# Performance work log

Hardware: AMD Instinct MI355X
Metric: run time of the kernel (lower is better)

## Reference

```python
import jax, jax.numpy as jnp
import numpy as np

B, LS, LT = 64, 64, 64
E, H = 512, 512
VS, VT = 32000, 32000


def setup_inputs() -> dict:
    key = jax.random.key(0)
    ks = jax.random.split(key, 16)
    s = 0.02
    inp = {
        "src": jax.random.randint(ks[0], (B, LS), 0, VS),
        "tgt": jax.random.randint(ks[1], (B, LT), 0, VT),
        # encoder params
        "src_embed": jax.random.normal(ks[2], (VS, E), jnp.float32) * s,
        "enc_Wx": jax.random.normal(ks[3], (E, 4 * H), jnp.float32) * s,   # [i|f|g|o]
        "enc_Wh": jax.random.normal(ks[4], (H, 4 * H), jnp.float32) * s,
        "enc_b": jnp.zeros((4 * H,), jnp.float32),
        # decoder params
        "tgt_embed": jax.random.normal(ks[5], (VT, E), jnp.float32) * s,
        "att_Wh": jax.random.normal(ks[6], (H, H), jnp.float32) * s,
        "att_Ws": jax.random.normal(ks[7], (H, H), jnp.float32) * s,
        "att_v": jax.random.normal(ks[8], (H,), jnp.float32) * s,
        "dec_Wx": jax.random.normal(ks[9], (E + H, 4 * H), jnp.float32) * s,
        "dec_Wh": jax.random.normal(ks[10], (H, 4 * H), jnp.float32) * s,
        "dec_b": jnp.zeros((4 * H,), jnp.float32),
        "h2o_W": jax.random.normal(ks[11], (2 * H, VT), jnp.float32) * s,
        "h2o_b": jnp.zeros((VT,), jnp.float32),
    }
    return inp


def _lstm_step(x, h, c, Wx, Wh, b):
    # x:(B,in), h,c:(B,H). Gates packed as [i|f|g|o] along last dim (same math
    # as 8 separate nn.Linear calls with biases summed).
    z = x @ Wx + h @ Wh + b
    i, f, g, o = jnp.split(z, 4, axis=-1)
    c_new = jax.nn.sigmoid(f) * c + jax.nn.sigmoid(i) * jnp.tanh(g)
    h_new = jax.nn.sigmoid(o) * jnp.tanh(c_new)
    return h_new, c_new


def reference(src, tgt, src_embed, enc_Wx, enc_Wh, enc_b, tgt_embed,
              att_Wh, att_Ws, att_v, dec_Wx, dec_Wh, dec_b, h2o_W, h2o_b):
    Bs = src.shape[0]
    h0 = jnp.zeros((Bs, H), jnp.float32)
    c0 = jnp.zeros((Bs, H), jnp.float32)

    # ---- encoder: scan over source timesteps ----
    src_emb = src_embed[src]                       # (B,Ls,E)
    xs_enc = jnp.swapaxes(src_emb, 0, 1)           # (Ls,B,E)

    def enc_step(carry, x):
        h, c = carry
        h, c = _lstm_step(x, h, c, enc_Wx, enc_Wh, enc_b)
        return (h, c), h

    (h_enc, c_enc), enc_hs = jax.lax.scan(enc_step, (h0, c0), xs_enc)
    enc_hiddens = jnp.swapaxes(enc_hs, 0, 1)       # (B,Ls,H)

    # encoder-side attention projection is decoder-state independent: hoist it
    enc_t = enc_hiddens @ att_Wh                   # (B,Ls,H)

    # ---- decoder: teacher forcing, scan over target timesteps ----
    tgt_emb = tgt_embed[tgt]                       # (B,Lt,E)
    xs_dec = jnp.swapaxes(tgt_emb, 0, 1)           # (Lt,B,E)

    def dec_step(carry, emb):
        h, c = carry
        # Bahdanau additive attention on previous decoder hidden h
        dec_t = h @ att_Ws                                        # (B,H)
        energy = jnp.tanh(enc_t + dec_t[:, None, :]) @ att_v      # (B,Ls)
        attn = jax.nn.softmax(energy, axis=-1)                    # (B,Ls)
        context = jnp.einsum('bs,bsh->bh', attn, enc_hiddens)     # (B,H)
        lstm_in = jnp.concatenate([emb, context], axis=-1)        # (B,E+H)
        h, c = _lstm_step(lstm_in, h, c, dec_Wx, dec_Wh, dec_b)
        logits = jnp.concatenate([h, context], axis=-1) @ h2o_W + h2o_b
        out = jax.nn.log_softmax(logits, axis=-1)                 # (B,Vt)
        return (h, c), out

    _, outs = jax.lax.scan(dec_step, (h_enc, c_enc), xs_dec)      # (Lt,B,Vt)
    return jnp.swapaxes(outs, 0, 1)                               # (B,Lt,Vt)
```

## Files before the change

kernel.cpp:

```cpp
#include <hip/hip_runtime.h>
#include <hip/hip_bf16.h>
#include <math.h>

#define BB 64
#define LL 64
#define EE 512
#define HH 512
#define G4 2048
#define VT 32000
#define RT 4096

typedef unsigned short u16;
typedef unsigned int u32;
typedef unsigned char u8;
typedef __attribute__((ext_vector_type(2))) unsigned int u32x2;
typedef __attribute__((ext_vector_type(8))) unsigned short ushort8;
typedef __attribute__((ext_vector_type(8))) short bf16x8;
typedef __attribute__((ext_vector_type(4))) float f32x4;

__device__ u16   gW2T[(size_t)VT * 1024];
__device__ u16   gEncWxT[G4 * EE];
__device__ u16   gEncWhT[G4 * HH];
__device__ u16   gAttWhT[HH * HH];
__device__ u16   gDecWxTe[G4 * EE];
__device__ u16   gDecWxTc[G4 * HH];
__device__ u16   gDecWhT[G4 * HH];
__device__ u8    gWs8[HH * HH];
__device__ u16   gSrcEmb[RT * EE];
__device__ u16   gTgtEmb[RT * EE];
__device__ float gXWxE[(size_t)RT * G4];
__device__ float gXWxD[(size_t)RT * G4];
__device__ u16   gEncHb[(size_t)RT * HH];
__device__ u16   gEncHb2[(size_t)RT * HH];
__device__ u16   gEncTb[(size_t)RT * HH];
__device__ u16   gHcat[(size_t)RT * 1024];
__device__ float gC[BB * HH];
__device__ float gAv[HH];
__device__ unsigned gFlagE[64];
__device__ unsigned gFlagB[64];
__device__ unsigned gFlagC[64];
__device__ unsigned gStep;

__device__ __forceinline__ u16 f2b(float f) {
    union { float f; unsigned u; } v{f};
    unsigned r = v.u + 0x7fffu + ((v.u >> 16) & 1u);
    return (u16)(r >> 16);
}
__device__ __forceinline__ float b2f(u16 x) {
    union { unsigned u; float f; } v; v.u = ((unsigned)x) << 16; return v.f;
}
__device__ __forceinline__ float sigm(float x) { return 1.f / (1.f + __expf(-x)); }
__device__ __forceinline__ float ftanh(float x) {
    x = fminf(15.f, fmaxf(-15.f, x));
    float e = __expf(2.f * x);
    return (e - 1.f) / (e + 1.f);
}

__device__ unsigned char encf8(float f) {
    union { float f; unsigned u; } v{f};
    unsigned s = (v.u >> 31) << 7;
    float af = fabsf(f);
    if (af < 0.0009765625f) return (unsigned char)s;
    if (af >= 448.f) return (unsigned char)(s | 0x7E);
    if (af < 0.015625f) {
        int q = (int)rintf(af * 512.f);
        if (q >= 8) return (unsigned char)(s | 0x08);
        return (unsigned char)(s | q);
    }
    int e; float m = frexpf(af, &e);
    int E = e - 1 + 7;
    int q = (int)rintf((m * 2.f - 1.f) * 8.f);
    if (q == 8) { E++; q = 0; }
    if (E >= 15) return (unsigned char)(s | 0x7E);
    return (unsigned char)(s | (E << 3) | q);
}
__device__ __forceinline__ float decf8s(unsigned v) {
    unsigned s = v >> 7, e = (v >> 3) & 15, m = v & 7;
    float mag = e ? ldexpf((float)(8 + m), (int)e - 10) : ldexpf((float)m, -9);
    return s ? -mag : mag;
}
#if __has_builtin(__builtin_amdgcn_cvt_f32_fp8)
#define DEC8(w, sel) __builtin_amdgcn_cvt_f32_fp8((int)(w), sel)
#else
#define DEC8(w, sel) decf8s(((w) >> (8 * (sel))) & 0xFFu)
#endif

__device__ __forceinline__ void ld16(const void* addr, bf16x8* a) {
    asm volatile(
        "global_load_dwordx4 %0, %16, off sc0 sc1\n\t"
        "global_load_dwordx4 %1, %16, off offset:64 sc0 sc1\n\t"
        "global_load_dwordx4 %2, %16, off offset:128 sc0 sc1\n\t"
        "global_load_dwordx4 %3, %16, off offset:192 sc0 sc1\n\t"
        "global_load_dwordx4 %4, %16, off offset:256 sc0 sc1\n\t"
        "global_load_dwordx4 %5, %16, off offset:320 sc0 sc1\n\t"
        "global_load_dwordx4 %6, %16, off offset:384 sc0 sc1\n\t"
        "global_load_dwordx4 %7, %16, off offset:448 sc0 sc1\n\t"
        "global_load_dwordx4 %8, %16, off offset:512 sc0 sc1\n\t"
        "global_load_dwordx4 %9, %16, off offset:576 sc0 sc1\n\t"
        "global_load_dwordx4 %10, %16, off offset:640 sc0 sc1\n\t"
        "global_load_dwordx4 %11, %16, off offset:704 sc0 sc1\n\t"
        "global_load_dwordx4 %12, %16, off offset:768 sc0 sc1\n\t"
        "global_load_dwordx4 %13, %16, off offset:832 sc0 sc1\n\t"
        "global_load_dwordx4 %14, %16, off offset:896 sc0 sc1\n\t"
        "global_load_dwordx4 %15, %16, off offset:960 sc0 sc1\n\t"
        "s_waitcnt vmcnt(0)"
        : "=&v"(a[0]), "=&v"(a[1]), "=&v"(a[2]), "=&v"(a[3]),
          "=&v"(a[4]), "=&v"(a[5]), "=&v"(a[6]), "=&v"(a[7]),
          "=&v"(a[8]), "=&v"(a[9]), "=&v"(a[10]), "=&v"(a[11]),
          "=&v"(a[12]), "=&v"(a[13]), "=&v"(a[14]), "=&v"(a[15])
        : "v"(addr) : "memory");
}
__device__ __forceinline__ u32 ld1(const void* addr) {
    u32 r;
    asm volatile("global_load_dword %0, %1, off sc0 sc1\n\ts_waitcnt vmcnt(0)"
                 : "=&v"(r) : "v"(addr) : "memory");
    return r;
}
__device__ __forceinline__ void st8b(void* p, u32x2 v) {
    asm volatile("global_store_dwordx2 %0, %1, off sc0 sc1" :: "v"(p), "v"(v) : "memory");
}
__device__ __forceinline__ void st32b(u32* p, u32 v) {
    asm volatile("global_store_dword %0, %1, off sc0 sc1" :: "v"(p), "v"(v) : "memory");
}

__device__ __forceinline__ void setflag(unsigned* f, unsigned v) {
    asm volatile("s_waitcnt vmcnt(0)" ::: "memory");
    __syncthreads();
    if (threadIdx.x == 0) st32b((u32*)f, v);
}
__device__ __forceinline__ void waitflags(unsigned* flags, int n, unsigned target) {
    if (threadIdx.x < 64) {
        const unsigned* p = flags + (threadIdx.x & (n - 1));
        for (;;) {
            u32 v = ld1(p);
            if (__all(v >= target)) break;
            __builtin_amdgcn_s_sleep(1);
        }
    }
    __syncthreads();
}

__device__ __forceinline__ void g2l16(const u16* g, u16* l) {
    __builtin_amdgcn_global_load_lds(
        (const __attribute__((address_space(1))) unsigned int*)g,
        (__attribute__((address_space(3))) unsigned int*)l, 16, 0, 0);
}
__device__ __forceinline__ void g2l16nt(const u16* g, u16* l) {
    __builtin_amdgcn_global_load_lds(
        (const __attribute__((address_space(1))) unsigned int*)g,
        (__attribute__((address_space(3))) unsigned int*)l, 16, 0, 2);
}

__device__ inline u16* bf16sel(int s) {
    switch (s) {
        case 1: return gEncWxT; case 2: return gEncWhT;
        case 3: return gAttWhT; case 4: return gDecWxTe; case 5: return gDecWxTc;
        default: return gDecWhT;
    }
}

__global__ __launch_bounds__(256) void k_transpose(const float* __restrict__ in, int R, int C, int sel) {
    __shared__ float tile[32][33];
    int tx = threadIdx.x & 31, ty0 = threadIdx.x >> 5;
    int c0 = blockIdx.x * 32, r0 = blockIdx.y * 32;
#pragma unroll
    for (int k = 0; k < 4; k++) {
        int ty = ty0 + k * 8;
        tile[ty][tx] = in[(size_t)(r0 + ty) * C + c0 + tx];
    }
    __syncthreads();
    u16* out = bf16sel(sel);
#pragma unroll
    for (int k = 0; k < 4; k++) {
        int ty = ty0 + k * 8;
        out[(size_t)(c0 + ty) * R + r0 + tx] = f2b(tile[tx][ty]);
    }
}

__global__ __launch_bounds__(256) void k_tofp8(const float* __restrict__ in) {
    int i = blockIdx.x * 256 + threadIdx.x;
    gWs8[i] = encf8(in[i]);
}

__global__ __launch_bounds__(256) void k_gather(const int* __restrict__ tok, const float* __restrict__ tab, int sel) {
    int r = blockIdx.x;
    int b = r & 63, t = r >> 6;
    int token = tok[b * LL + t];
    u16* dst = (sel == 0) ? gSrcEmb : gTgtEmb;
    const float* srow = tab + (size_t)token * EE;
    for (int e = threadIdx.x; e < EE; e += 256)
        dst[(size_t)r * EE + e] = f2b(srow[e]);
}

__global__ __launch_bounds__(256) void k_zero() {
    int i = blockIdx.x * 256 + threadIdx.x;
    gC[i] = 0.f;
    if (i < 64) st32b((u32*)(gFlagE + i), 0u);
}

__global__ __launch_bounds__(256) void k_rst(const float* __restrict__ av) {
    int t = threadIdx.x;
    gAv[t] = av[t];
    gAv[t + 256] = av[t + 256];
    if (t < 64) {
        st32b((u32*)(gFlagB + t), 0u);
        st32b((u32*)(gFlagC + t), 0u);
    }
    if (t == 0) st32b((u32*)&gStep, 0u);
}

__global__ __launch_bounds__(256) void k_gemm(int selA, int lda, int selB, int ldb,
                                              int M, int N, int K, int epi,
                                              const float* __restrict__ bias, int selOut) {
    __shared__ u16 sA[128 * 72];
    __shared__ u16 sB[128 * 72];
    const u16* Ag = (selA == 0) ? gSrcEmb : gEncHb;
    const u16* Bg = (selB == 0) ? gEncWxT : gAttWhT;
    float* Cg = gXWxE;

    int tid = threadIdx.x, l = tid & 63, wid = tid >> 6, wr = wid >> 1, wc = wid & 1;
    int ar = l & 15, ak = (l >> 4) * 8;
    int rowM = blockIdx.y * 128, colN = blockIdx.x * 128;
    f32x4 acc[4][4];
#pragma unroll
    for (int m = 0; m < 4; m++)
#pragma unroll
        for (int n = 0; n < 4; n++) acc[m][n] = (f32x4){0.f, 0.f, 0.f, 0.f};

    for (int k0 = 0; k0 < K; k0 += 64) {
#pragma unroll
        for (int it = 0; it < 4; it++) {
            int idx = it * 256 + tid;
            int row = idx >> 3, cc = idx & 7;
            *(ushort8*)(sA + row * 72 + cc * 8) =
                *(const ushort8*)(Ag + (size_t)(rowM + row) * lda + k0 + cc * 8);
            *(ushort8*)(sB + row * 72 + cc * 8) =
                *(const ushort8*)(Bg + (size_t)(colN + row) * ldb + k0 + cc * 8);
        }
        __syncthreads();
#pragma unroll
        for (int ks = 0; ks < 2; ks++) {
            bf16x8 a[4], b[4];
#pragma unroll
            for (int m = 0; m < 4; m++) a[m] = *(const bf16x8*)(sA + (wr * 64 + m * 16 + ar) * 72 + ks * 32 + ak);
#pragma unroll
            for (int n = 0; n < 4; n++) b[n] = *(const bf16x8*)(sB + (wc * 64 + n * 16 + ar) * 72 + ks * 32 + ak);
#pragma unroll
            for (int m = 0; m < 4; m++)
#pragma unroll
                for (int n = 0; n < 4; n++)
                    acc[m][n] = __builtin_amdgcn_mfma_f32_16x16x32_bf16(a[m], b[n], acc[m][n], 0, 0, 0);
        }
        __syncthreads();
    }
    int rb = (l >> 4) * 4;
#pragma unroll
    for (int m = 0; m < 4; m++)
#pragma unroll
        for (int n = 0; n < 4; n++)
#pragma unroll
            for (int ri = 0; ri < 4; ri++) {
                int row = rowM + wr * 64 + m * 16 + rb + ri;
                int col = colN + wc * 64 + n * 16 + ar;
                float v = acc[m][n][ri];
                if (epi == 2) Cg[(size_t)row * N + col] = v + bias[col];
                else gEncTb[(size_t)((row & 63) * 64 + (row >> 6)) * N + col] = f2b(v);
            }
}

__global__ __launch_bounds__(256) void k_encoder(const float* __restrict__ dec_b,
                                                 const float* __restrict__ h2o_W) {
    __shared__ char smem[67584];
    int tid = threadIdx.x, l = tid & 63, wid = tid >> 6;
    int bx = blockIdx.x;
    int ar = l & 15, ak = (l >> 4) * 8, rb = (l >> 4) * 4;
    if (bx < 32) {
        u16* sW = (u16*)smem;
        u16* s_hout = (u16*)(smem + 65536);
        int j = bx;
#pragma unroll
        for (int it = 0; it < 16; it++) {
            int idx = it * 256 + tid;
            int lr = idx >> 6, kc = idx & 63;
            int gcol = (lr >> 4) * 512 + j * 16 + (lr & 15);
            int off = (lr * 1024 + kc * 16) ^ ((lr & 7) << 4);
            *(ushort8*)((char*)sW + off) = *(const ushort8*)(gEncWhT + (size_t)gcol * 512 + kc * 8);
        }
        __syncthreads();
        int arow = wid * 16 + ar, aoff = (l >> 4) * 16;
        int hcol = j * 16 + ar;
        for (int t = 0; t < LL; t++) {
            float xwv[4][4];
#pragma unroll
            for (int ri = 0; ri < 4; ri++) {
                const float* xw = gXWxE + (size_t)(t * BB + wid * 16 + rb + ri) * G4;
#pragma unroll
                for (int g = 0; g < 4; g++) xwv[ri][g] = xw[g * 512 + hcol];
            }
            f32x4 acc[4];
#pragma unroll
            for (int g = 0; g < 4; g++) acc[g] = (f32x4){0.f, 0.f, 0.f, 0.f};
            if (t > 0) {
                waitflags(gFlagE, 32, (unsigned)t);
                bf16x8 af[16];
                ld16((const char*)gEncHb + (size_t)((t - 1) * BB + arow) * 1024 + aoff, af);
#pragma unroll
                for (int kk = 0; kk < 16; kk++) {
                    int k = kk * 32 + ak;
#pragma unroll
                    for (int g = 0; g < 4; g++) {
                        int lr = g * 16 + ar;
                        bf16x8 b = *(const bf16x8*)((char*)sW + ((lr * 1024 + k * 2) ^ ((lr & 7) << 4)));
                        acc[g] = __builtin_amdgcn_mfma_f32_16x16x32_bf16(af[kk], b, acc[g], 0, 0, 0);
                    }
                }
            }
#pragma unroll
            for (int ri = 0; ri < 4; ri++) {
                int row = wid * 16 + rb + ri;
                float zi = acc[0][ri] + xwv[ri][0];
                float zf = acc[1][ri] + xwv[ri][1];
                float zg = acc[2][ri] + xwv[ri][2];
                float zo = acc[3][ri] + xwv[ri][3];
                float co = gC[row * HH + hcol];
                float cn = sigm(zf) * co + sigm(zi) * ftanh(zg);
                float hn = sigm(zo) * ftanh(cn);
                gC[row * HH + hcol] = cn;
                s_hout[row * 16 + ar] = f2b(hn);
            }
            __syncthreads();
            {
                int row = tid >> 2, seg = tid & 3;
                u32x2 v = *(const u32x2*)(s_hout + row * 16 + seg * 4);
                st8b(gEncHb + (size_t)(t * BB + row) * HH + j * 16 + seg * 4, v);
                *(u32x2*)(gEncHb2 + (size_t)(row * LL + t) * HH + j * 16 + seg * 4) = v;
            }
            setflag(gFlagE + j, (unsigned)(t + 1));
        }
    } else if (bx < 96) {
        u16* sA = (u16*)smem;
        u16* sB = (u16*)(smem + 18432);
        int wr = wid >> 1, wc = wid & 1;
        for (int it8 = 0; it8 < 8; it8++) {
            int ti = (bx - 32) * 8 + it8;
            int bxx = ti & 15, byy = ti >> 4;
            int rowM = byy * 128, colN = bxx * 128;
            f32x4 acc[4][4];
#pragma unroll
            for (int m = 0; m < 4; m++)
#pragma unroll
                for (int n = 0; n < 4; n++) acc[m][n] = (f32x4){0.f, 0.f, 0.f, 0.f};
            for (int k0 = 0; k0 < 512; k0 += 64) {
#pragma unroll
                for (int it = 0; it < 4; it++) {
                    int idx = it * 256 + tid;
                    int row = idx >> 3, cc = idx & 7;
                    *(ushort8*)(sA + row * 72 + cc * 8) =
                        *(const ushort8*)(gTgtEmb + (size_t)(rowM + row) * 512 + k0 + cc * 8);
                    *(ushort8*)(sB + row * 72 + cc * 8) =
                        *(const ushort8*)(gDecWxTe + (size_t)(colN + row) * 512 + k0 + cc * 8);
                }
                __syncthreads();
#pragma unroll
                for (int ks = 0; ks < 2; ks++) {
                    bf16x8 a[4], b[4];
#pragma unroll
                    for (int m = 0; m < 4; m++) a[m] = *(const bf16x8*)(sA + (wr * 64 + m * 16 + ar) * 72 + ks * 32 + ak);
#pragma unroll
                    for (int n = 0; n < 4; n++) b[n] = *(const bf16x8*)(sB + (wc * 64 + n * 16 + ar) * 72 + ks * 32 + ak);
#pragma unroll
                    for (int m = 0; m < 4; m++)
#pragma unroll
                        for (int n = 0; n < 4; n++)
                            acc[m][n] = __builtin_amdgcn_mfma_f32_16x16x32_bf16(a[m], b[n], acc[m][n], 0, 0, 0);
                }
                __syncthreads();
            }
#pragma unroll
            for (int m = 0; m < 4; m++)
#pragma unroll
                for (int n = 0; n < 4; n++)
#pragma unroll
                    for (int ri = 0; ri < 4; ri++) {
                        int row = rowM + wr * 64 + m * 16 + rb + ri;
                        int col = colN + wc * 64 + n * 16 + ar;
                        gXWxD[(size_t)row * G4 + col] = acc[m][n][ri] + dec_b[col];
                    }
        }
    } else {
        float (*tile)[33] = (float(*)[33])smem;
        int tx = tid & 31, ty0 = tid >> 5;
        for (int k = 0; k < 200; k++) {
            int ti = (bx - 96) * 200 + k;
            int ct = ti % 1000, rt = ti / 1000;
            int c0 = ct * 32, r0 = rt * 32;
            __syncthreads();
#pragma unroll
            for (int kk = 0; kk < 4; kk++) {
                int ty = ty0 + kk * 8;
                tile[ty][tx] = h2o_W[(size_t)(r0 + ty) * VT + c0 + tx];
            }
            __syncthreads();
#pragma unroll
            for (int kk = 0; kk < 4; kk++) {
                int ty = ty0 + kk * 8;
                gW2T[(size_t)(c0 + ty) * 1024 + r0 + tx] = f2b(tile[tx][ty]);
            }
        }
    }
}

__global__ __launch_bounds__(256) void k_decoder(const float* __restrict__ h2o_b,
                                                 float* __restrict__ out) {
    __shared__ u16 sWh[64 * 512];
    __shared__ u16 sWx[64 * 512];
    __shared__ u16 s_hout[64 * 16];
    __shared__ float s_h[512];
    __shared__ float s_dt[512];
    __shared__ float s_av[512];
    __shared__ float s_att[64];
    __shared__ float s_red[256];
    __shared__ float s_mv[4][520];
    int tid = threadIdx.x, l = tid & 63, wid = tid >> 6;
    int bx = blockIdx.x;
    int ar = l & 15, ak = (l >> 4) * 8, rb = (l >> 4) * 4;
    int arow = wid * 16 + ar, aoff = (l >> 4) * 16;
    if (bx >= 96) {
        u16* csA = sWh;
        u16* csB = sWh + 128 * 64;
        int wr = wid >> 1, wc = wid & 1;
        int srow = wid * 32 + (l >> 3);
        int scol = (l & 7) * 8;
        int ci = bx - 96;
        for (int jt = 0; jt < 50; jt++) {
            int T = ci + 160 * jt;
            int byy = T / 250, bxx = T % 250;
            unsigned tgt = (unsigned)(2 * byy + 2);
            if (tid == 0) {
                while (ld1(&gStep) < tgt) __builtin_amdgcn_s_sleep(32);
            }
            __syncthreads();
            int rowM = byy * 128, colN = bxx * 128;
            f32x4 acc[4][4];
#pragma unroll
            for (int m = 0; m < 4; m++)
#pragma unroll
                for (int n = 0; n < 4; n++) acc[m][n] = (f32x4){0.f, 0.f, 0.f, 0.f};
            for (int k0 = 0; k0 < 1024; k0 += 64) {
#pragma unroll
                for (int c = 0; c < 4; c++) {
                    int r = srow + c * 8;
                    g2l16(gHcat + (size_t)(rowM + r) * 1024 + k0 + scol, csA + r * 64 + scol);
                    g2l16nt(gW2T + (size_t)(colN + r) * 1024 + k0 + scol, csB + r * 64 + scol);
                }
                __syncthreads();
#pragma unroll
                for (int ks = 0; ks < 2; ks++) {
                    bf16x8 a[4], b[4];
#pragma unroll
                    for (int m = 0; m < 4; m++) a[m] = *(const bf16x8*)(csA + (wr * 64 + m * 16 + ar) * 64 + ks * 32 + ak);
#pragma unroll
                    for (int n = 0; n < 4; n++) b[n] = *(const bf16x8*)(csB + (wc * 64 + n * 16 + ar) * 64 + ks * 32 + ak);
#pragma unroll
                    for (int m = 0; m < 4; m++)
#pragma unroll
                        for (int n = 0; n < 4; n++)
                            acc[m][n] = __builtin_amdgcn_mfma_f32_16x16x32_bf16(a[m], b[n], acc[m][n], 0, 0, 0);
                }
                __syncthreads();
            }
#pragma unroll
            for (int m = 0; m < 4; m++)
#pragma unroll
                for (int n = 0; n < 4; n++)
#pragma unroll
                    for (int ri = 0; ri < 4; ri++) {
                        int row = rowM + wr * 64 + m * 16 + rb + ri;
                        int col = colN + wc * 64 + n * 16 + ar;
                        out[(size_t)((row & 63) * 64 + (row >> 6)) * VT + col] = acc[m][n][ri] + h2o_b[col];
                    }
        }
        return;
    }
    if (bx >= 64) {
        int j = bx - 64;
#pragma unroll
        for (int it = 0; it < 16; it++) {
            int idx = it * 256 + tid;
            int lr = idx >> 6, kc = idx & 63;
            int gcol = (lr >> 4) * 512 + j * 16 + (lr & 15);
            int off = (lr * 1024 + kc * 16) ^ ((lr & 7) << 4);
            *(ushort8*)((char*)sWh + off) = *(const ushort8*)(gDecWhT + (size_t)gcol * 512 + kc * 8);
            *(ushort8*)((char*)sWx + off) = *(const ushort8*)(gDecWxTc + (size_t)gcol * 512 + kc * 8);
        }
    } else {
        s_av[tid] = gAv[tid];
        s_av[tid + 256] = gAv[tid + 256];
    }
    __syncthreads();
    for (int t = 0; t < LL; t++) {
        if (bx >= 64) {
            int j = bx - 64;
            int hcol = j * 16 + ar;
            float xwv[4][4];
#pragma unroll
            for (int ri = 0; ri < 4; ri++) {
                const float* xw = gXWxD + (size_t)(t * BB + wid * 16 + rb + ri) * G4;
#pragma unroll
                for (int g = 0; g < 4; g++) xwv[ri][g] = xw[g * 512 + hcol];
            }
            if (t > 0) waitflags(gFlagC, 32, (unsigned)t);
            if (t > 0 && bx == 64 && tid == 0) st32b((u32*)&gStep, (unsigned)t);
            bf16x8 af[16];
            const char* baseA = (t == 0)
                ? ((const char*)gEncHb + (size_t)(63 * BB + arow) * 1024 + aoff)
                : ((const char*)gHcat + (size_t)((t - 1) * BB + arow) * 2048 + aoff);
            ld16(baseA, af);
            f32x4 acc[4];
#pragma unroll
            for (int g = 0; g < 4; g++) acc[g] = (f32x4){0.f, 0.f, 0.f, 0.f};
#pragma unroll
            for (int kk = 0; kk < 16; kk++) {
                int k = kk * 32 + ak;
#pragma unroll
                for (int g = 0; g < 4; g++) {
                    int lr = g * 16 + ar;
                    bf16x8 b = *(const bf16x8*)((char*)sWh + ((lr * 1024 + k * 2) ^ ((lr & 7) << 4)));
                    acc[g] = __builtin_amdgcn_mfma_f32_16x16x32_bf16(af[kk], b, acc[g], 0, 0, 0);
                }
            }
            waitflags(gFlagB, 64, (unsigned)(t + 1));
            bf16x8 cf[16];
            ld16((const char*)gHcat + (size_t)(t * BB + arow) * 2048 + 1024 + aoff, cf);
#pragma unroll
            for (int kk = 0; kk < 16; kk++) {
                int k = kk * 32 + ak;
#pragma unroll
                for (int g = 0; g < 4; g++) {
                    int lr = g * 16 + ar;
                    bf16x8 b = *(const bf16x8*)((char*)sWx + ((lr * 1024 + k * 2) ^ ((lr & 7) << 4)));
                    acc[g] = __builtin_amdgcn_mfma_f32_16x16x32_bf16(cf[kk], b, acc[g], 0, 0, 0);
                }
            }
#pragma unroll
            for (int ri = 0; ri < 4; ri++) {
                int row = wid * 16 + rb + ri;
                float zi = acc[0][ri] + xwv[ri][0];
                float zf = acc[1][ri] + xwv[ri][1];
                float zg = acc[2][ri] + xwv[ri][2];
                float zo = acc[3][ri] + xwv[ri][3];
                float co = gC[row * HH + hcol];
                float cn = sigm(zf) * co + sigm(zi) * ftanh(zg);
                float hn = sigm(zo) * ftanh(cn);
                gC[row * HH + hcol] = cn;
                s_hout[row * 16 + ar] = f2b(hn);
            }
            __syncthreads();
            {
                int row = tid >> 2, seg = tid & 3;
                u32x2 v = *(const u32x2*)(s_hout + row * 16 + seg * 4);
                st8b(gHcat + (size_t)(t * BB + row) * 1024 + j * 16 + seg * 4, v);
            }
            setflag(gFlagC + j, (unsigned)(t + 1));
        } else {
            int b = bx;
            if (t > 0) waitflags(gFlagC, 32, (unsigned)t);
            const char* hb = (t == 0) ? ((const char*)gEncHb + (size_t)(63 * BB + b) * 1024)
                                      : ((const char*)gHcat + (size_t)((t - 1) * BB + b) * 2048);
            u32 hw = ld1(hb + 4 * tid);
            s_h[2 * tid] = b2f((u16)(hw & 0xffff));
            s_h[2 * tid + 1] = b2f((u16)(hw >> 16));
            __syncthreads();
            {
                int c8 = tid & 63, kq = tid >> 6;
                float a8[8];
#pragma unroll
                for (int jj = 0; jj < 8; jj++) a8[jj] = 0.f;
                const u8* wp = gWs8 + (size_t)(kq * 128) * 512 + c8 * 8;
#pragma unroll 4
                for (int i = 0; i < 128; i++) {
                    u32x2 w = *(const u32x2*)(wp + (size_t)i * 512);
                    float hk = s_h[kq * 128 + i];
                    a8[0] += hk * DEC8(w.x, 0);
                    a8[1] += hk * DEC8(w.x, 1);
                    a8[2] += hk * DEC8(w.x, 2);
                    a8[3] += hk * DEC8(w.x, 3);
                    a8[4] += hk * DEC8(w.y, 0);
                    a8[5] += hk * DEC8(w.y, 1);
                    a8[6] += hk * DEC8(w.y, 2);
                    a8[7] += hk * DEC8(w.y, 3);
                }
#pragma unroll
                for (int jj = 0; jj < 8; jj++) s_mv[kq][c8 * 8 + jj] = a8[jj];
            }
            __syncthreads();
            s_dt[tid] = s_mv[0][tid] + s_mv[1][tid] + s_mv[2][tid] + s_mv[3][tid];
            s_dt[tid + 256] = s_mv[0][tid + 256] + s_mv[1][tid + 256] + s_mv[2][tid + 256] + s_mv[3][tid + 256];
            __syncthreads();
            {
                int s = tid >> 2, q = tid & 3;
                const u16* et = gEncTb + (size_t)(b * 64 + s) * 512 + q * 128;
                const float* dtp = s_dt + q * 128;
                const float* avp = s_av + q * 128;
                float p = 0.f;
#pragma unroll
                for (int i = 0; i < 16; i++) {
                    ushort8 ev = *(const ushort8*)(et + i * 8);
#pragma unroll
                    for (int jj = 0; jj < 8; jj++) {
                        int h = i * 8 + jj;
                        p += ftanh(b2f((u16)ev[jj]) + dtp[h]) * avp[h];
                    }
                }
                s_red[tid] = p;
            }
            __syncthreads();
            if (tid < 64) {
                float v = s_red[tid * 4] + s_red[tid * 4 + 1] + s_red[tid * 4 + 2] + s_red[tid * 4 + 3];
                float m = v;
                for (int o = 32; o; o >>= 1) m = fmaxf(m, __shfl_xor(m, o));
                float e = __expf(v - m);
                float ss = e;
                for (int o = 32; o; o >>= 1) ss += __shfl_xor(ss, o);
                s_att[tid] = e / ss;
            }
            __syncthreads();
            int c = tid * 2;
            float c0 = 0.f, c1 = 0.f;
            const u16* eh = gEncHb2 + (size_t)b * LL * HH;
#pragma unroll 8
            for (int s2 = 0; s2 < 64; s2++) {
                float a = s_att[s2];
                u32 w = *(const u32*)(eh + (size_t)s2 * HH + c);
                c0 += a * b2f((u16)(w & 0xffff));
                c1 += a * b2f((u16)(w >> 16));
            }
            u32 cw = (u32)f2b(c0) | ((u32)f2b(c1) << 16);
            st32b((u32*)(gHcat + (size_t)(t * BB + b) * 1024 + 512 + c), cw);
            setflag(gFlagB + b, (unsigned)(t + 1));
        }
    }
    if (bx == 64) {
        waitflags(gFlagC, 32, 64u);
        waitflags(gFlagB, 64, 64u);
        if (tid == 0) st32b((u32*)&gStep, 64u);
    }
}

__global__ __launch_bounds__(256) void k_lsm(float* __restrict__ out) {
    int row = blockIdx.x, tid = threadIdx.x;
    float4* p4 = (float4*)(out + (size_t)row * VT);
    float m = -1e30f, s = 0.f;
    for (int i = tid; i < VT / 4; i += 256) {
        float4 v = p4[i];
        float mx = fmaxf(fmaxf(v.x, v.y), fmaxf(v.z, v.w));
        float mn = fmaxf(m, mx);
        s = s * __expf(m - mn) + __expf(v.x - mn) + __expf(v.y - mn) + __expf(v.z - mn) + __expf(v.w - mn);
        m = mn;
    }
    for (int o = 32; o; o >>= 1) {
        float m2 = __shfl_xor(m, o), s2 = __shfl_xor(s, o);
        float mn = fmaxf(m, m2);
        s = s * __expf(m - mn) + s2 * __expf(m2 - mn);
        m = mn;
    }
    __shared__ float rm[4], rs[4];
    if ((tid & 63) == 0) { rm[tid >> 6] = m; rs[tid >> 6] = s; }
    __syncthreads();
    float mm = fmaxf(fmaxf(rm[0], rm[1]), fmaxf(rm[2], rm[3]));
    float ss = rs[0] * __expf(rm[0] - mm) + rs[1] * __expf(rm[1] - mm) +
               rs[2] * __expf(rm[2] - mm) + rs[3] * __expf(rm[3] - mm);
    float lse = mm + __logf(ss);
    for (int i = tid; i < VT / 4; i += 256) {
        float4 v = p4[i];
        v.x -= lse; v.y -= lse; v.z -= lse; v.w -= lse;
        p4[i] = v;
    }
}

extern "C" void kernel_launch(void* const* d_in, const int* in_sizes, int n_in,
                              void* d_out, int out_size, void* d_ws, size_t ws_size,
                              hipStream_t stream) {
    const int*   src       = (const int*)d_in[0];
    const int*   tgt       = (const int*)d_in[1];
    const float* src_embed = (const float*)d_in[2];
    const float* enc_Wx    = (const float*)d_in[3];
    const float* enc_Wh    = (const float*)d_in[4];
    const float* enc_b     = (const float*)d_in[5];
    const float* tgt_embed = (const float*)d_in[6];
    const float* att_Wh    = (const float*)d_in[7];
    const float* att_Ws    = (const float*)d_in[8];
    const float* att_v     = (const float*)d_in[9];
    const float* dec_Wx    = (const float*)d_in[10];
    const float* dec_Wh    = (const float*)d_in[11];
    const float* dec_b     = (const float*)d_in[12];
    const float* h2o_W     = (const float*)d_in[13];
    const float* h2o_b     = (const float*)d_in[14];
    float* out = (float*)d_out;
    dim3 blk(256);

    k_transpose<<<dim3(G4 / 32, EE / 32), blk, 0, stream>>>(enc_Wx, EE, G4, 1);
    k_transpose<<<dim3(G4 / 32, HH / 32), blk, 0, stream>>>(enc_Wh, HH, G4, 2);
    k_transpose<<<dim3(HH / 32, HH / 32), blk, 0, stream>>>(att_Wh, HH, HH, 3);
    k_transpose<<<dim3(G4 / 32, EE / 32), blk, 0, stream>>>(dec_Wx, EE, G4, 4);
    k_transpose<<<dim3(G4 / 32, HH / 32), blk, 0, stream>>>(dec_Wx + (size_t)512 * G4, HH, G4, 5);
    k_transpose<<<dim3(G4 / 32, HH / 32), blk, 0, stream>>>(dec_Wh, HH, G4, 6);
    k_tofp8<<<HH * HH / 256, blk, 0, stream>>>(att_Ws);
    k_gather<<<RT, blk, 0, stream>>>(src, src_embed, 0);
    k_gather<<<RT, blk, 0, stream>>>(tgt, tgt_embed, 1);
    k_zero<<<128, blk, 0, stream>>>();
    k_gemm<<<dim3(G4 / 128, RT / 128), blk, 0, stream>>>(0, 512, 0, 512, RT, G4, 512, 2, enc_b, 0);
    const float* decb = dec_b;
    const float* h2ow = h2o_W;
    void* eargs[] = { (void*)&decb, (void*)&h2ow };
    hipLaunchCooperativeKernel((const void*)k_encoder, dim3(256), dim3(256), eargs, 0, stream);
    k_gemm<<<dim3(HH / 128, RT / 128), blk, 0, stream>>>(2, 512, 2, 512, RT, HH, 512, 4, nullptr, 2);
    k_rst<<<1, blk, 0, stream>>>(att_v);
    const float* h2ob = h2o_b;
    float* outp = out;
    void* dargs[] = { (void*)&h2ob, (void*)&outp };
    hipLaunchCooperativeKernel((const void*)k_decoder, dim3(256), dim3(256), dargs, 0, stream);
    k_lsm<<<RT, blk, 0, stream>>>(out);
}
```

Measured before the change: 2.774 ms.

## Split decoder recurrence into two independent batch halves with separate flag groups

The decoder LSTM blocks are split into two groups of 32, each handling 32 batch rows, so the two batch halves proceed independently, each with its own flags and step counter. Gate results go through shared memory so every thread computes two cells. Attention blocks wait only on their own half's flags. The output GEMM now uses 128 blocks instead of 160 and waits on both step counters. The aim is to shorten the per-step critical path through narrower synchronization, at the cost of fewer GEMM workers and more flag traffic.

```diff
diff --git a/kernel.cpp b/kernel.cpp
--- a/kernel.cpp
+++ b/kernel.cpp
@@ -40,6 +40,7 @@
 __device__ unsigned gFlagB[64];
 __device__ unsigned gFlagC[64];
 __device__ unsigned gStep;
+__device__ unsigned gStep2;
 
 __device__ __forceinline__ u16 f2b(float f) {
     union { float f; unsigned u; } v{f};
@@ -206,7 +207,7 @@
         st32b((u32*)(gFlagB + t), 0u);
         st32b((u32*)(gFlagC + t), 0u);
     }
-    if (t == 0) st32b((u32*)&gStep, 0u);
+    if (t == 0) { st32b((u32*)&gStep, 0u); st32b((u32*)&gStep2, 0u); }
 }
 
 __global__ __launch_bounds__(256) void k_gemm(int selA, int lda, int selB, int ldb,
@@ -414,7 +415,8 @@
                                                  float* __restrict__ out) {
     __shared__ u16 sWh[64 * 512];
     __shared__ u16 sWx[64 * 512];
-    __shared__ u16 s_hout[64 * 16];
+    __shared__ float s_z[4][32][17];
+    __shared__ u16 s_hout[32 * 16];
     __shared__ float s_h[512];
     __shared__ float s_dt[512];
     __shared__ float s_av[512];
@@ -424,20 +426,22 @@
     int tid = threadIdx.x, l = tid & 63, wid = tid >> 6;
     int bx = blockIdx.x;
     int ar = l & 15, ak = (l >> 4) * 8, rb = (l >> 4) * 4;
-    int arow = wid * 16 + ar, aoff = (l >> 4) * 16;
-    if (bx >= 96) {
+    int aoff = (l >> 4) * 16;
+    if (bx >= 128) {
         u16* csA = sWh;
         u16* csB = sWh + 128 * 64;
         int wr = wid >> 1, wc = wid & 1;
         int srow = wid * 32 + (l >> 3);
         int scol = (l & 7) * 8;
-        int ci = bx - 96;
-        for (int jt = 0; jt < 50; jt++) {
-            int T = ci + 160 * jt;
+        int ci = bx - 128;
+        for (int jt = 0; jt < 63; jt++) {
+            int T = ci + 128 * jt;
+            if (T >= 8000) break;
             int byy = T / 250, bxx = T % 250;
             unsigned tgt = (unsigned)(2 * byy + 2);
             if (tid == 0) {
                 while (ld1(&gStep) < tgt) __builtin_amdgcn_s_sleep(32);
+                while (ld1(&gStep2) < tgt) __builtin_amdgcn_s_sleep(32);
             }
             __syncthreads();
             int rowM = byy * 128, colN = bxx * 128;
@@ -483,7 +487,8 @@
         return;
     }
     if (bx >= 64) {
-        int j = bx - 64;
+        int c = (bx - 64) >> 5, j = (bx - 64) & 31, cb = 32 * c;
+        int mt = wid & 1, gp = wid >> 1;
 #pragma unroll
         for (int it = 0; it < 16; it++) {
             int idx = it * 256 + tid;
@@ -493,80 +498,105 @@
             *(ushort8*)((char*)sWh + off) = *(const ushort8*)(gDecWhT + (size_t)gcol * 512 + kc * 8);
             *(ushort8*)((char*)sWx + off) = *(const ushort8*)(gDecWxTc + (size_t)gcol * 512 + kc * 8);
         }
-    } else {
+        __syncthreads();
+        int cell0 = tid, cell1 = tid + 256;
+        int r30 = cell0 >> 4, hc0 = cell0 & 15;
+        int r31 = cell1 >> 4, hc1 = cell1 & 15;
+        int arow2 = cb + mt * 16 + ar;
+        for (int t = 0; t < LL; t++) {
+            float xwv[2][4];
+            const float* xw0 = gXWxD + (size_t)(t * 64 + cb + r30) * G4;
+            const float* xw1 = gXWxD + (size_t)(t * 64 + cb + r31) * G4;
+#pragma unroll
+            for (int g = 0; g < 4; g++) {
+                xwv[0][g] = xw0[g * 512 + 16 * j + hc0];
+                xwv[1][g] = xw1[g * 512 + 16 * j + hc1];
+            }
+            if (t > 0) waitflags(gFlagC + cb, 32, (unsigned)t);
+            if (t > 0 && j == 0 && tid == 0)
+                st32b(c ? (u32*)&gStep2 : (u32*)&gStep, (unsigned)t);
+            bf16x8 af[16];
+            const char* baseA = (t == 0)
+                ? ((const char*)gEncHb + (size_t)(63 * 64 + arow2) * 1024 + aoff)
+                : ((const char*)gHcat + (size_t)((t - 1) * 64 + arow2) * 2048 + aoff);
+            ld16(baseA, af);
+            f32x4 acc[2];
+            acc[0] = (f32x4){0.f, 0.f, 0.f, 0.f};
+            acc[1] = (f32x4){0.f, 0.f, 0.f, 0.f};
+#pragma unroll
+            for (int kk = 0; kk < 16; kk++) {
+                int k = kk * 32 + ak;
+#pragma unroll
+                for (int gi = 0; gi < 2; gi++) {
+                    int lr = (2 * gp + gi) * 16 + ar;
+                    bf16x8 b = *(const bf16x8*)((char*)sWh + ((lr * 1024 + k * 2) ^ ((lr & 7) << 4)));
+                    acc[gi] = __builtin_amdgcn_mfma_f32_16x16x32_bf16(af[kk], b, acc[gi], 0, 0, 0);
+                }
+            }
+            waitflags(gFlagB + cb, 32, (unsigned)(t + 1));
+            bf16x8 cf[16];
+            ld16((const char*)gHcat + (size_t)(t * 64 + arow2) * 2048 + 1024 + aoff, cf);
+#pragma unroll
+            for (int kk = 0; kk < 16; kk++) {
+                int k = kk * 32 + ak;
+#pragma unroll
+                for (int gi = 0; gi < 2; gi++) {
+                    int lr = (2 * gp + gi) * 16 + ar;
+                    bf16x8 b = *(const bf16x8*)((char*)sWx + ((lr * 1024 + k * 2) ^ ((lr & 7) << 4)));
+                    acc[gi] = __builtin_amdgcn_mfma_f32_16x16x32_bf16(cf[kk], b, acc[gi], 0, 0, 0);
+                }
+            }
+#pragma unroll
+            for (int gi = 0; gi < 2; gi++)
+#pragma unroll
+                for (int ri = 0; ri < 4; ri++)
+                    s_z[2 * gp + gi][mt * 16 + rb + ri][ar] = acc[gi][ri];
+            __syncthreads();
+            {
+                float zi = s_z[0][r30][hc0] + xwv[0][0];
+                float zf = s_z[1][r30][hc0] + xwv[0][1];
+                float zg = s_z[2][r30][hc0] + xwv[0][2];
+                float zo = s_z[3][r30][hc0] + xwv[0][3];
+                float co = gC[(cb + r30) * HH + 16 * j + hc0];
+                float cn = sigm(zf) * co + sigm(zi) * ftanh(zg);
+                float hn = sigm(zo) * ftanh(cn);
+                gC[(cb + r30) * HH + 16 * j + hc0] = cn;
+                s_hout[r30 * 16 + hc0] = f2b(hn);
+                zi = s_z[0][r31][hc1] + xwv[1][0];
+                zf = s_z[1][r31][hc1] + xwv[1][1];
+                zg = s_z[2][r31][hc1] + xwv[1][2];
+                zo = s_z[3][r31][hc1] + xwv[1][3];
+                co = gC[(cb + r31) * HH + 16 * j + hc1];
+                cn = sigm(zf) * co + sigm(zi) * ftanh(zg);
+                hn = sigm(zo) * ftanh(cn);
+                gC[(cb + r31) * HH + 16 * j + hc1] = cn;
+                s_hout[r31 * 16 + hc1] = f2b(hn);
+            }
+            __syncthreads();
+            if (tid < 128) {
+                int row = tid >> 2, seg = tid & 3;
+                u32x2 v = *(const u32x2*)(s_hout + row * 16 + seg * 4);
+                st8b(gHcat + (size_t)(t * 64 + cb + row) * 1024 + j * 16 + seg * 4, v);
+            }
+            setflag(gFlagC + cb + j, (unsigned)(t + 1));
+        }
+        if (j == 0) {
+            waitflags(gFlagC + cb, 32, 64u);
+            waitflags(gFlagB + cb, 32, 64u);
+            if (tid == 0) st32b(c ? (u32*)&gStep2 : (u32*)&gStep, 64u);
+        }
+        return;
+    }
+    {
+        int b = bx;
+        int cb = (b >> 5) << 5;
         s_av[tid] = gAv[tid];
         s_av[tid + 256] = gAv[tid + 256];
-    }
-    __syncthreads();
-    for (int t = 0; t < LL; t++) {
-        if (bx >= 64) {
-            int j = bx - 64;
-            int hcol = j * 16 + ar;
-            float xwv[4][4];
-#pragma unroll
-            for (int ri = 0; ri < 4; ri++) {
-                const float* xw = gXWxD + (size_t)(t * BB + wid * 16 + rb + ri) * G4;
-#pragma unroll
-                for (int g = 0; g < 4; g++) xwv[ri][g] = xw[g * 512 + hcol];
-            }
-            if (t > 0) waitflags(gFlagC, 32, (unsigned)t);
-            if (t > 0 && bx == 64 && tid == 0) st32b((u32*)&gStep, (unsigned)t);
-            bf16x8 af[16];
-            const char* baseA = (t == 0)
-                ? ((const char*)gEncHb + (size_t)(63 * BB + arow) * 1024 + aoff)
-                : ((const char*)gHcat + (size_t)((t - 1) * BB + arow) * 2048 + aoff);
-            ld16(baseA, af);
-            f32x4 acc[4];
-#pragma unroll
-            for (int g = 0; g < 4; g++) acc[g] = (f32x4){0.f, 0.f, 0.f, 0.f};
-#pragma unroll
-            for (int kk = 0; kk < 16; kk++) {
-                int k = kk * 32 + ak;
-#pragma unroll
-                for (int g = 0; g < 4; g++) {
-                    int lr = g * 16 + ar;
-                    bf16x8 b = *(const bf16x8*)((char*)sWh + ((lr * 1024 + k * 2) ^ ((lr & 7) << 4)));
-                    acc[g] = __builtin_amdgcn_mfma_f32_16x16x32_bf16(af[kk], b, acc[g], 0, 0, 0);
-                }
-            }
-            waitflags(gFlagB, 64, (unsigned)(t + 1));
-            bf16x8 cf[16];
-            ld16((const char*)gHcat + (size_t)(t * BB + arow) * 2048 + 1024 + aoff, cf);
-#pragma unroll
-            for (int kk = 0; kk < 16; kk++) {
-                int k = kk * 32 + ak;
-#pragma unroll
-                for (int g = 0; g < 4; g++) {
-                    int lr = g * 16 + ar;
-                    bf16x8 b = *(const bf16x8*)((char*)sWx + ((lr * 1024 + k * 2) ^ ((lr & 7) << 4)));
-                    acc[g] = __builtin_amdgcn_mfma_f32_16x16x32_bf16(cf[kk], b, acc[g], 0, 0, 0);
-                }
-            }
-#pragma unroll
-            for (int ri = 0; ri < 4; ri++) {
-                int row = wid * 16 + rb + ri;
-                float zi = acc[0][ri] + xwv[ri][0];
-                float zf = acc[1][ri] + xwv[ri][1];
-                float zg = acc[2][ri] + xwv[ri][2];
-                float zo = acc[3][ri] + xwv[ri][3];
-                float co = gC[row * HH + hcol];
-                float cn = sigm(zf) * co + sigm(zi) * ftanh(zg);
-                float hn = sigm(zo) * ftanh(cn);
-                gC[row * HH + hcol] = cn;
-                s_hout[row * 16 + ar] = f2b(hn);
-            }
-            __syncthreads();
-            {
-                int row = tid >> 2, seg = tid & 3;
-                u32x2 v = *(const u32x2*)(s_hout + row * 16 + seg * 4);
-                st8b(gHcat + (size_t)(t * BB + row) * 1024 + j * 16 + seg * 4, v);
-            }
-            setflag(gFlagC + j, (unsigned)(t + 1));
-        } else {
-            int b = bx;
-            if (t > 0) waitflags(gFlagC, 32, (unsigned)t);
-            const char* hb = (t == 0) ? ((const char*)gEncHb + (size_t)(63 * BB + b) * 1024)
-                                      : ((const char*)gHcat + (size_t)((t - 1) * BB + b) * 2048);
+        __syncthreads();
+        for (int t = 0; t < LL; t++) {
+            if (t > 0) waitflags(gFlagC + cb, 32, (unsigned)t);
+            const char* hb = (t == 0) ? ((const char*)gEncHb + (size_t)(63 * 64 + b) * 1024)
+                                      : ((const char*)gHcat + (size_t)((t - 1) * 64 + b) * 2048);
             u32 hw = ld1(hb + 4 * tid);
             s_h[2 * tid] = b2f((u16)(hw & 0xffff));
             s_h[2 * tid + 1] = b2f((u16)(hw >> 16));
@@ -636,14 +666,9 @@
                 c1 += a * b2f((u16)(w >> 16));
             }
             u32 cw = (u32)f2b(c0) | ((u32)f2b(c1) << 16);
-            st32b((u32*)(gHcat + (size_t)(t * BB + b) * 1024 + 512 + c), cw);
+            st32b((u32*)(gHcat + (size_t)(t * 64 + b) * 1024 + 512 + c), cw);
             setflag(gFlagB + b, (unsigned)(t + 1));
         }
-    }
-    if (bx == 64) {
-        waitflags(gFlagC, 32, 64u);
-        waitflags(gFlagB, 64, 64u);
-        if (tid == 0) st32b((u32*)&gStep, 64u);
     }
 }
 
```

Measured after the change: 3.039 ms. +9.6%, slower.
